# Kernel optimization log

Measured on AMD Instinct MI355X. Metric: run time of the kernel, lower is better.

## Reference

```python
import jax, jax.numpy as jnp
import numpy as np

B, N, IN_F, OUT_F, H = 64, 256, 128, 128, 4
NEG_SLOPE = 0.2  # nn.LeakyReLU(dropout) -> slope 0.2


def setup_inputs() -> dict:
    key = jax.random.key(0)
    ks = jax.random.split(key, 10)
    h = jax.random.normal(ks[0], (B, N, IN_F), dtype=jnp.float32)
    projection_matrix = jax.random.normal(ks[1], (B, N, N), dtype=jnp.float32)
    similarity_matrix = jax.random.uniform(ks[2], (B, N, N), dtype=jnp.float32) * 2.0 - 1.0
    quadrant_matrix = jax.random.randint(ks[3], (B, N, N, 2), 0, 4, dtype=jnp.int32)
    # parameters (xavier-ish scaling)
    W = jax.random.normal(ks[4], (IN_F, OUT_F * H), dtype=jnp.float32) / np.sqrt(IN_F)
    a = jax.random.normal(ks[5], (H, 2 * OUT_F, 1), dtype=jnp.float32) / np.sqrt(2 * OUT_F)
    w_proj = jax.random.normal(ks[6], (OUT_F,), dtype=jnp.float32) / np.sqrt(OUT_F)
    w_sim = jax.random.normal(ks[7], (OUT_F,), dtype=jnp.float32) / np.sqrt(OUT_F)
    quadrant_bias = jax.random.normal(ks[8], (4, 4), dtype=jnp.float32) * 0.02
    W_concat = jax.random.normal(ks[9], (OUT_F * H, OUT_F), dtype=jnp.float32) / np.sqrt(OUT_F * H)
    return {"h": h, "projection_matrix": projection_matrix,
            "similarity_matrix": similarity_matrix, "quadrant_matrix": quadrant_matrix,
            "W": W, "a": a, "w_proj": w_proj, "w_sim": w_sim,
            "quadrant_bias": quadrant_bias, "W_concat": W_concat}


def reference(h, projection_matrix, similarity_matrix, quadrant_matrix,
              W, a, w_proj, w_sim, quadrant_bias, W_concat):
    b, n, _ = h.shape
    # Wh_heads: (B, H, N, F)
    Wh = (h @ W).reshape(b, n, H, OUT_F).transpose(0, 2, 1, 3)
    # GAT score: a^T [Wh_i || Wh_j] decomposes into two rank-1 terms
    a1, a2 = a[:, :OUT_F, 0], a[:, OUT_F:, 0]            # (H, F) each
    e_i = jnp.einsum('bhnf,hf->bhn', Wh, a1)
    e_j = jnp.einsum('bhnf,hf->bhn', Wh, a2)
    e = e_i[:, :, :, None] + e_j[:, :, None, :]          # (B, H, N, N)
    e = jnp.where(e > 0, e, NEG_SLOPE * e)               # leaky relu
    # projection bias: <Wh_i, proj[b,i,j] * w_proj> = (Wh_i . w_proj) * proj[b,i,j]
    s_proj = jnp.einsum('bhnf,f->bhn', Wh, w_proj)
    e = e + s_proj[:, :, :, None] * projection_matrix[:, None, :, :]
    # similarity bias, same factored form
    s_sim = jnp.einsum('bhnf,f->bhn', Wh, w_sim)
    e = e + s_sim[:, :, :, None] * similarity_matrix[:, None, :, :]
    # quadrant bias gather
    qb = quadrant_bias[quadrant_matrix[..., 0], quadrant_matrix[..., 1]]  # (B, N, N)
    e = e + qb[:, None, :, :]
    attn = jax.nn.softmax(e, axis=-1)                    # dropout is identity in eval
    h_prime = jnp.einsum('bhij,bhjf->bhif', attn, Wh)    # (B, H, N, F)
    h_prime = h_prime.transpose(0, 2, 1, 3).reshape(b, n, H * OUT_F) @ W_concat
    return jax.nn.elu(h_prime)
```

## Files before the change

### kernel.cpp

```cpp
#include <hip/hip_runtime.h>
#include <math.h>

#define BB 64
#define NN 256
#define IN_F 128
#define OF 128
#define HH 4
#define NEG_SLOPE 0.2f

typedef __attribute__((ext_vector_type(8))) short short8;
typedef __attribute__((ext_vector_type(4))) float f32x4;

#define MFMA16(a, b, c) __builtin_amdgcn_mfma_f32_16x16x32_bf16(a, b, c, 0, 0, 0)

__device__ inline unsigned short f2bf(float x) {
    unsigned u = __float_as_uint(x);
    u += 0x7fff + ((u >> 16) & 1);
    return (unsigned short)(u >> 16);
}

__global__ __launch_bounds__(256) void k0_convert(const float* __restrict__ h,
        const float* __restrict__ W, const float* __restrict__ Wc,
        unsigned short* __restrict__ h_bf, unsigned short* __restrict__ Wt,
        unsigned short* __restrict__ Wct) {
    int blk = blockIdx.x, t = threadIdx.x;
    if (blk < 2048) {
        int idx = blk * 256 + t;
        float4 v = ((const float4*)h)[idx];
        ushort4 o;
        o.x = f2bf(v.x); o.y = f2bf(v.y); o.z = f2bf(v.z); o.w = f2bf(v.w);
        ((ushort4*)h_bf)[idx] = o;
    } else if (blk < 2064) {
        int base = (blk - 2048) * 4096 + t * 16;
#pragma unroll
        for (int e = 0; e < 16; e++) {
            int idx = base + e;
            int f = idx >> 7, k = idx & 127;
            Wt[idx] = f2bf(W[k * 512 + f]);
        }
    } else {
        int base = (blk - 2064) * 4096 + t * 16;
#pragma unroll
        for (int e = 0; e < 16; e++) {
            int idx = base + e;
            int c = idx >> 9, k = idx & 511;
            Wct[idx] = f2bf(Wc[k * 128 + c]);
        }
    }
}

__global__ __launch_bounds__(256) void k1_wh(const unsigned short* __restrict__ h_bf,
        const unsigned short* __restrict__ Wt, const float* __restrict__ a,
        const float* __restrict__ w_proj, const float* __restrict__ w_sim,
        unsigned short* __restrict__ Wht, float* __restrict__ ei,
        float* __restrict__ ej, float* __restrict__ sp, float* __restrict__ ss) {
    __shared__ float a1s[512], a2s[512], wps[128], wss[128];
    int blk = blockIdx.x;
    int b = blk >> 2;
    int n0 = (blk & 3) * 64;
    int t = threadIdx.x;
    for (int idx = t; idx < 512; idx += 256) {
        int hh = idx >> 7, f = idx & 127;
        a1s[idx] = a[hh * 256 + f];
        a2s[idx] = a[hh * 256 + 128 + f];
    }
    if (t < 128) { wps[t] = w_proj[t]; wss[t] = w_sim[t]; }
    __syncthreads();

    int w = t >> 6, lane = t & 63;
    int cc = lane & 15, g = lane >> 4;

    short8 bh[4][4];
#pragma unroll
    for (int tn = 0; tn < 4; tn++)
#pragma unroll
        for (int ks = 0; ks < 4; ks++)
            bh[tn][ks] = *(const short8*)(h_bf +
                ((size_t)(b * NN + n0 + tn * 16 + cc)) * IN_F + ks * 32 + g * 8);

    f32x4 acc[8][4];
#pragma unroll
    for (int tf = 0; tf < 8; tf++)
#pragma unroll
        for (int tn = 0; tn < 4; tn++) acc[tf][tn] = (f32x4)(0.f);

#pragma unroll
    for (int tf = 0; tf < 8; tf++) {
        short8 aw[4];
#pragma unroll
        for (int ks = 0; ks < 4; ks++)
            aw[ks] = *(const short8*)(Wt +
                (size_t)(w * 128 + tf * 16 + cc) * IN_F + ks * 32 + g * 8);
#pragma unroll
        for (int tn = 0; tn < 4; tn++)
#pragma unroll
            for (int ks = 0; ks < 4; ks++)
                acc[tf][tn] = MFMA16(aw[ks], bh[tn][ks], acc[tf][tn]);
    }

    unsigned short* whb = Wht + (size_t)(b * HH + w) * OF * NN;
#pragma unroll
    for (int tf = 0; tf < 8; tf++)
#pragma unroll
        for (int r = 0; r < 4; r++) {
            int f = tf * 16 + g * 4 + r;
#pragma unroll
            for (int tn = 0; tn < 4; tn++)
                whb[(size_t)f * NN + n0 + tn * 16 + cc] = f2bf(acc[tf][tn][r]);
        }

#pragma unroll
    for (int tn = 0; tn < 4; tn++) {
        float q0 = 0.f, q1 = 0.f, q2 = 0.f, q3 = 0.f;
#pragma unroll
        for (int tf = 0; tf < 8; tf++)
#pragma unroll
            for (int r = 0; r < 4; r++) {
                float v = acc[tf][tn][r];
                int f = tf * 16 + g * 4 + r;
                q0 += v * a1s[w * 128 + f];
                q1 += v * a2s[w * 128 + f];
                q2 += v * wps[f];
                q3 += v * wss[f];
            }
        q0 += __shfl_xor(q0, 16); q0 += __shfl_xor(q0, 32);
        q1 += __shfl_xor(q1, 16); q1 += __shfl_xor(q1, 32);
        q2 += __shfl_xor(q2, 16); q2 += __shfl_xor(q2, 32);
        q3 += __shfl_xor(q3, 16); q3 += __shfl_xor(q3, 32);
        if (g == 0) {
            size_t idx = (size_t)(b * HH + w) * NN + n0 + tn * 16 + cc;
            ei[idx] = q0; ej[idx] = q1; sp[idx] = q2; ss[idx] = q3;
        }
    }
}

__global__ __launch_bounds__(256) void k2_fused(
        const float* __restrict__ proj, const float* __restrict__ sim,
        const int* __restrict__ qm, const float* __restrict__ qbias,
        const float* __restrict__ ei, const float* __restrict__ ej,
        const float* __restrict__ sp, const float* __restrict__ ss,
        const unsigned short* __restrict__ Wht, const unsigned short* __restrict__ Wct,
        float* __restrict__ out) {
    __shared__ __align__(16) char at_lds[32768];
    __shared__ __align__(16) char hp_lds[16384];
    __shared__ float eis[HH][16], sps[HH][16], sss[HH][16];
    __shared__ float qb_s[16];
    float* ejs = (float*)hp_lds;

    int blk = blockIdx.x;
    int b = blk >> 4;
    int i0 = (blk & 15) * 16;
    int t = threadIdx.x;
    int wave = t >> 6, lane = t & 63;

    for (int c = t; c < HH * NN; c += 256)
        ejs[c] = ej[(size_t)b * HH * NN + c];
    if (t < 64) {
        int hh = t >> 4, ii = t & 15;
        size_t base = ((size_t)b * HH + hh) * NN + i0 + ii;
        eis[hh][ii] = ei[base]; sps[hh][ii] = sp[base]; sss[hh][ii] = ss[base];
    }
    if (t < 16) qb_s[t] = qbias[t];
    __syncthreads();

    int j0 = lane * 4;
    for (int rr = 0; rr < 4; rr++) {
        int ii = wave * 4 + rr;
        int i = i0 + ii;
        size_t rb = ((size_t)b * NN + i) * NN + j0;
        float4 P4 = *(const float4*)&proj[rb];
        float4 S4 = *(const float4*)&sim[rb];
        int4 q0 = *(const int4*)&qm[rb * 2];
        int4 q1 = *(const int4*)&qm[rb * 2 + 4];
        float qb0 = qb_s[q0.x * 4 + q0.y], qb1 = qb_s[q0.z * 4 + q0.w];
        float qb2 = qb_s[q1.x * 4 + q1.y], qb3 = qb_s[q1.z * 4 + q1.w];
        float e[HH][4];
#pragma unroll
        for (int hh = 0; hh < HH; hh++) {
            float4 ej4 = *(const float4*)&ejs[hh * 256 + j0];
            float bi = eis[hh][ii], spv = sps[hh][ii], ssv = sss[hh][ii];
            float x;
            x = bi + ej4.x; x = x > 0.f ? x : NEG_SLOPE * x; e[hh][0] = x + spv * P4.x + ssv * S4.x + qb0;
            x = bi + ej4.y; x = x > 0.f ? x : NEG_SLOPE * x; e[hh][1] = x + spv * P4.y + ssv * S4.y + qb1;
            x = bi + ej4.z; x = x > 0.f ? x : NEG_SLOPE * x; e[hh][2] = x + spv * P4.z + ssv * S4.z + qb2;
            x = bi + ej4.w; x = x > 0.f ? x : NEG_SLOPE * x; e[hh][3] = x + spv * P4.w + ssv * S4.w + qb3;
        }
        float m[HH];
#pragma unroll
        for (int hh = 0; hh < HH; hh++)
            m[hh] = fmaxf(fmaxf(e[hh][0], e[hh][1]), fmaxf(e[hh][2], e[hh][3]));
#pragma unroll
        for (int off = 32; off; off >>= 1)
#pragma unroll
            for (int hh = 0; hh < HH; hh++)
                m[hh] = fmaxf(m[hh], __shfl_xor(m[hh], off));
        float s[HH];
#pragma unroll
        for (int hh = 0; hh < HH; hh++) {
            e[hh][0] = __expf(e[hh][0] - m[hh]);
            e[hh][1] = __expf(e[hh][1] - m[hh]);
            e[hh][2] = __expf(e[hh][2] - m[hh]);
            e[hh][3] = __expf(e[hh][3] - m[hh]);
            s[hh] = (e[hh][0] + e[hh][1]) + (e[hh][2] + e[hh][3]);
        }
#pragma unroll
        for (int off = 32; off; off >>= 1)
#pragma unroll
            for (int hh = 0; hh < HH; hh++) s[hh] += __shfl_xor(s[hh], off);
#pragma unroll
        for (int hh = 0; hh < HH; hh++) {
            float inv = 1.0f / s[hh];
            ushort4 pk;
            pk.x = f2bf(e[hh][0] * inv);
            pk.y = f2bf(e[hh][1] * inv);
            pk.z = f2bf(e[hh][2] * inv);
            pk.w = f2bf(e[hh][3] * inv);
            int off2 = hh * 8192 + ii * 512 + ((j0 * 2) ^ ((ii & 7) << 4));
            *(ushort4*)(at_lds + off2) = pk;
        }
    }
    __syncthreads();

    int w = wave;
    int row = lane & 15, g = lane >> 4;
    short8 af[8];
#pragma unroll
    for (int ks = 0; ks < 8; ks++) {
        int off = w * 8192 + row * 512 + ((((ks * 32 + g * 8) * 2)) ^ ((row & 7) << 4));
        af[ks] = *(const short8*)(at_lds + off);
    }
    f32x4 acc[8];
#pragma unroll
    for (int ft = 0; ft < 8; ft++) acc[ft] = (f32x4)(0.f);
    const unsigned short* whb = Wht + (size_t)(b * HH + w) * OF * NN;
#pragma unroll
    for (int ft = 0; ft < 8; ft++) {
        const unsigned short* wb = whb + (size_t)(ft * 16 + row) * NN + g * 8;
#pragma unroll
        for (int ks = 0; ks < 8; ks++) {
            short8 bf = *(const short8*)(wb + ks * 32);
            acc[ft] = MFMA16(af[ks], bf, acc[ft]);
        }
    }
#pragma unroll
    for (int ft = 0; ft < 8; ft++)
#pragma unroll
        for (int r = 0; r < 4; r++) {
            int i = g * 4 + r;
            int kf = w * 128 + ft * 16 + row;
            int off = i * 1024 + ((kf * 2) ^ ((i & 7) << 4));
            *(unsigned short*)(hp_lds + off) = f2bf(acc[ft][r]);
        }
    __syncthreads();

    short8 ah[16];
#pragma unroll
    for (int ks = 0; ks < 16; ks++) {
        int off = row * 1024 + (((ks * 32 + g * 8) * 2) ^ ((row & 7) << 4));
        ah[ks] = *(const short8*)(hp_lds + off);
    }
    f32x4 o2[2];
    o2[0] = (f32x4)(0.f); o2[1] = (f32x4)(0.f);
#pragma unroll
    for (int ct = 0; ct < 2; ct++) {
        int c = (w * 2 + ct) * 16 + row;
        const unsigned short* wc = Wct + (size_t)c * 512 + g * 8;
#pragma unroll
        for (int ks = 0; ks < 16; ks++) {
            short8 bf = *(const short8*)(wc + ks * 32);
            o2[ct] = MFMA16(ah[ks], bf, o2[ct]);
        }
    }
#pragma unroll
    for (int ct = 0; ct < 2; ct++)
#pragma unroll
        for (int r = 0; r < 4; r++) {
            float v = o2[ct][r];
            v = v > 0.f ? v : expm1f(v);
            int i = i0 + g * 4 + r;
            int c = (w * 2 + ct) * 16 + row;
            out[((size_t)b * NN + i) * OF + c] = v;
        }
}

extern "C" void kernel_launch(void* const* d_in, const int* in_sizes, int n_in,
                              void* d_out, int out_size, void* d_ws, size_t ws_size,
                              hipStream_t stream) {
    const float* h      = (const float*)d_in[0];
    const float* proj   = (const float*)d_in[1];
    const float* sim    = (const float*)d_in[2];
    const int*   qm     = (const int*)d_in[3];
    const float* W      = (const float*)d_in[4];
    const float* a      = (const float*)d_in[5];
    const float* w_proj = (const float*)d_in[6];
    const float* w_sim  = (const float*)d_in[7];
    const float* qbias  = (const float*)d_in[8];
    const float* Wc     = (const float*)d_in[9];
    float* out = (float*)d_out;

    unsigned short* h_bf = (unsigned short*)d_ws;
    unsigned short* Wt   = h_bf + (size_t)BB * NN * IN_F;
    unsigned short* Wct  = Wt + 512 * 128;
    unsigned short* Wht  = Wct + 128 * 512;
    float* ei = (float*)(Wht + (size_t)BB * HH * OF * NN);
    float* ej = ei + (size_t)BB * HH * NN;
    float* sp = ej + (size_t)BB * HH * NN;
    float* ss = sp + (size_t)BB * HH * NN;

    k0_convert<<<2080, 256, 0, stream>>>(h, W, Wc, h_bf, Wt, Wct);
    k1_wh<<<BB * 4, 256, 0, stream>>>(h_bf, Wt, a, w_proj, w_sim, Wht, ei, ej, sp, ss);
    k2_fused<<<BB * 16, 256, 0, stream>>>(proj, sim, qm, qbias, ei, ej, sp, ss, Wht, Wct, out);
}
```

Before: 182.4 us.

## Coalesce weight transposes, remap blocks across XCDs, prefetch k2 inputs, shrink k1 registers

The weight transpose-convert in k0 now stages 16-row slabs of W and W_concat in shared memory. It then writes contiguous 16-element bf16 runs, replacing the strided scalar reads. k1 and k2 remap block indices so that all blocks for one batch land on the same XCD, which should improve L2 locality. k1 no longer keeps a full 8x4 accumulator array, computing the per-tile dot products and stores inside the tf loop, which lowers register pressure. k2 issues all four rows' proj/sim/quadrant loads up front to increase memory-level parallelism, at the cost of more live registers.

```diff
diff --git a/kernel.cpp b/kernel.cpp
--- a/kernel.cpp
+++ b/kernel.cpp
@@ -23,6 +23,7 @@
         const float* __restrict__ W, const float* __restrict__ Wc,
         unsigned short* __restrict__ h_bf, unsigned short* __restrict__ Wt,
         unsigned short* __restrict__ Wct) {
+    __shared__ float hl[16][516];
     int blk = blockIdx.x, t = threadIdx.x;
     if (blk < 2048) {
         int idx = blk * 256 + t;
@@ -30,21 +31,48 @@
         ushort4 o;
         o.x = f2bf(v.x); o.y = f2bf(v.y); o.z = f2bf(v.z); o.w = f2bf(v.w);
         ((ushort4*)h_bf)[idx] = o;
-    } else if (blk < 2064) {
-        int base = (blk - 2048) * 4096 + t * 16;
-#pragma unroll
-        for (int e = 0; e < 16; e++) {
-            int idx = base + e;
-            int f = idx >> 7, k = idx & 127;
-            Wt[idx] = f2bf(W[k * 512 + f]);
+    } else if (blk < 2056) {
+        int k0 = (blk - 2048) * 16;
+#pragma unroll
+        for (int it = 0; it < 8; it++) {
+            int li = it * 256 + t;
+            int row = li >> 7, col4 = li & 127;
+            float4 v = ((const float4*)(W + (size_t)(k0 + row) * 512))[col4];
+            *(float4*)&hl[row][col4 * 4] = v;
+        }
+        __syncthreads();
+#pragma unroll
+        for (int cc = 0; cc < 2; cc++) {
+            int c = t * 2 + cc;
+            short8 s0, s1;
+#pragma unroll
+            for (int k = 0; k < 8; k++) s0[k] = (short)f2bf(hl[k][c]);
+#pragma unroll
+            for (int k = 0; k < 8; k++) s1[k] = (short)f2bf(hl[k + 8][c]);
+            unsigned short* dst = Wt + (size_t)c * 128 + k0;
+            *(short8*)dst = s0;
+            *(short8*)(dst + 8) = s1;
         }
     } else {
-        int base = (blk - 2064) * 4096 + t * 16;
-#pragma unroll
-        for (int e = 0; e < 16; e++) {
-            int idx = base + e;
-            int c = idx >> 9, k = idx & 511;
-            Wct[idx] = f2bf(Wc[k * 128 + c]);
+        int k0 = (blk - 2056) * 16;
+#pragma unroll
+        for (int it = 0; it < 2; it++) {
+            int li = it * 256 + t;
+            int row = li >> 5, col4 = li & 31;
+            float4 v = ((const float4*)(Wc + (size_t)(k0 + row) * 128))[col4];
+            *(float4*)&hl[row][col4 * 4] = v;
+        }
+        __syncthreads();
+        if (t < 128) {
+            int c = t;
+            short8 s0, s1;
+#pragma unroll
+            for (int k = 0; k < 8; k++) s0[k] = (short)f2bf(hl[k][c]);
+#pragma unroll
+            for (int k = 0; k < 8; k++) s1[k] = (short)f2bf(hl[k + 8][c]);
+            unsigned short* dst = Wct + (size_t)c * 512 + k0;
+            *(short8*)dst = s0;
+            *(short8*)(dst + 8) = s1;
         }
     }
 }
@@ -55,9 +83,10 @@
         unsigned short* __restrict__ Wht, float* __restrict__ ei,
         float* __restrict__ ej, float* __restrict__ sp, float* __restrict__ ss) {
     __shared__ float a1s[512], a2s[512], wps[128], wss[128];
-    int blk = blockIdx.x;
-    int b = blk >> 2;
-    int n0 = (blk & 3) * 64;
+    int l = blockIdx.x;
+    int xcd = l & 7, m = l >> 3;
+    int b = xcd + ((m >> 2) << 3);
+    int n0 = (m & 3) * 64;
     int t = threadIdx.x;
     for (int idx = t; idx < 512; idx += 256) {
         int hh = idx >> 7, f = idx & 127;
@@ -78,11 +107,9 @@
             bh[tn][ks] = *(const short8*)(h_bf +
                 ((size_t)(b * NN + n0 + tn * 16 + cc)) * IN_F + ks * 32 + g * 8);
 
-    f32x4 acc[8][4];
-#pragma unroll
-    for (int tf = 0; tf < 8; tf++)
-#pragma unroll
-        for (int tn = 0; tn < 4; tn++) acc[tf][tn] = (f32x4)(0.f);
+    float q0[4] = {0.f,0.f,0.f,0.f}, q1[4] = {0.f,0.f,0.f,0.f};
+    float q2[4] = {0.f,0.f,0.f,0.f}, q3[4] = {0.f,0.f,0.f,0.f};
+    unsigned short* whb = Wht + (size_t)(b * HH + w) * OF * NN;
 
 #pragma unroll
     for (int tf = 0; tf < 8; tf++) {
@@ -91,45 +118,47 @@
         for (int ks = 0; ks < 4; ks++)
             aw[ks] = *(const short8*)(Wt +
                 (size_t)(w * 128 + tf * 16 + cc) * IN_F + ks * 32 + g * 8);
+        f32x4 acc[4];
+#pragma unroll
+        for (int tn = 0; tn < 4; tn++) acc[tn] = (f32x4)(0.f);
 #pragma unroll
         for (int tn = 0; tn < 4; tn++)
 #pragma unroll
             for (int ks = 0; ks < 4; ks++)
-                acc[tf][tn] = MFMA16(aw[ks], bh[tn][ks], acc[tf][tn]);
-    }
-
-    unsigned short* whb = Wht + (size_t)(b * HH + w) * OF * NN;
-#pragma unroll
-    for (int tf = 0; tf < 8; tf++)
+                acc[tn] = MFMA16(aw[ks], bh[tn][ks], acc[tn]);
+
+        float a1v[4], a2v[4], wpv[4], wsv[4];
 #pragma unroll
         for (int r = 0; r < 4; r++) {
             int f = tf * 16 + g * 4 + r;
-#pragma unroll
-            for (int tn = 0; tn < 4; tn++)
-                whb[(size_t)f * NN + n0 + tn * 16 + cc] = f2bf(acc[tf][tn][r]);
-        }
+            a1v[r] = a1s[w * 128 + f];
+            a2v[r] = a2s[w * 128 + f];
+            wpv[r] = wps[f];
+            wsv[r] = wss[f];
+        }
+#pragma unroll
+        for (int tn = 0; tn < 4; tn++)
+#pragma unroll
+            for (int r = 0; r < 4; r++) {
+                float v = acc[tn][r];
+                q0[tn] += v * a1v[r];
+                q1[tn] += v * a2v[r];
+                q2[tn] += v * wpv[r];
+                q3[tn] += v * wsv[r];
+                whb[(size_t)(tf * 16 + g * 4 + r) * NN + n0 + tn * 16 + cc] = f2bf(v);
+            }
+    }
 
 #pragma unroll
     for (int tn = 0; tn < 4; tn++) {
-        float q0 = 0.f, q1 = 0.f, q2 = 0.f, q3 = 0.f;
-#pragma unroll
-        for (int tf = 0; tf < 8; tf++)
-#pragma unroll
-            for (int r = 0; r < 4; r++) {
-                float v = acc[tf][tn][r];
-                int f = tf * 16 + g * 4 + r;
-                q0 += v * a1s[w * 128 + f];
-                q1 += v * a2s[w * 128 + f];
-                q2 += v * wps[f];
-                q3 += v * wss[f];
-            }
-        q0 += __shfl_xor(q0, 16); q0 += __shfl_xor(q0, 32);
-        q1 += __shfl_xor(q1, 16); q1 += __shfl_xor(q1, 32);
-        q2 += __shfl_xor(q2, 16); q2 += __shfl_xor(q2, 32);
-        q3 += __shfl_xor(q3, 16); q3 += __shfl_xor(q3, 32);
+        float p0 = q0[tn], p1 = q1[tn], p2 = q2[tn], p3 = q3[tn];
+        p0 += __shfl_xor(p0, 16); p0 += __shfl_xor(p0, 32);
+        p1 += __shfl_xor(p1, 16); p1 += __shfl_xor(p1, 32);
+        p2 += __shfl_xor(p2, 16); p2 += __shfl_xor(p2, 32);
+        p3 += __shfl_xor(p3, 16); p3 += __shfl_xor(p3, 32);
         if (g == 0) {
             size_t idx = (size_t)(b * HH + w) * NN + n0 + tn * 16 + cc;
-            ei[idx] = q0; ej[idx] = q1; sp[idx] = q2; ss[idx] = q3;
+            ei[idx] = p0; ej[idx] = p1; sp[idx] = p2; ss[idx] = p3;
         }
     }
 }
@@ -147,9 +176,10 @@
     __shared__ float qb_s[16];
     float* ejs = (float*)hp_lds;
 
-    int blk = blockIdx.x;
-    int b = blk >> 4;
-    int i0 = (blk & 15) * 16;
+    int l = blockIdx.x;
+    int xcd = l & 7, m = l >> 3;
+    int b = xcd + ((m >> 4) << 3);
+    int i0 = (m & 15) * 16;
     int t = threadIdx.x;
     int wave = t >> 6, lane = t & 63;
 
@@ -164,43 +194,49 @@
     __syncthreads();
 
     int j0 = lane * 4;
+    float4 P4[4], S4[4];
+    int4 qa[4], qc[4];
+#pragma unroll
+    for (int rr = 0; rr < 4; rr++) {
+        int i = i0 + wave * 4 + rr;
+        size_t rb = ((size_t)b * NN + i) * NN + j0;
+        P4[rr] = *(const float4*)&proj[rb];
+        S4[rr] = *(const float4*)&sim[rb];
+        qa[rr] = *(const int4*)&qm[rb * 2];
+        qc[rr] = *(const int4*)&qm[rb * 2 + 4];
+    }
+#pragma unroll
     for (int rr = 0; rr < 4; rr++) {
         int ii = wave * 4 + rr;
-        int i = i0 + ii;
-        size_t rb = ((size_t)b * NN + i) * NN + j0;
-        float4 P4 = *(const float4*)&proj[rb];
-        float4 S4 = *(const float4*)&sim[rb];
-        int4 q0 = *(const int4*)&qm[rb * 2];
-        int4 q1 = *(const int4*)&qm[rb * 2 + 4];
-        float qb0 = qb_s[q0.x * 4 + q0.y], qb1 = qb_s[q0.z * 4 + q0.w];
-        float qb2 = qb_s[q1.x * 4 + q1.y], qb3 = qb_s[q1.z * 4 + q1.w];
+        float qb0 = qb_s[qa[rr].x * 4 + qa[rr].y], qb1 = qb_s[qa[rr].z * 4 + qa[rr].w];
+        float qb2 = qb_s[qc[rr].x * 4 + qc[rr].y], qb3 = qb_s[qc[rr].z * 4 + qc[rr].w];
         float e[HH][4];
 #pragma unroll
         for (int hh = 0; hh < HH; hh++) {
             float4 ej4 = *(const float4*)&ejs[hh * 256 + j0];
             float bi = eis[hh][ii], spv = sps[hh][ii], ssv = sss[hh][ii];
             float x;
-            x = bi + ej4.x; x = x > 0.f ? x : NEG_SLOPE * x; e[hh][0] = x + spv * P4.x + ssv * S4.x + qb0;
-            x = bi + ej4.y; x = x > 0.f ? x : NEG_SLOPE * x; e[hh][1] = x + spv * P4.y + ssv * S4.y + qb1;
-            x = bi + ej4.z; x = x > 0.f ? x : NEG_SLOPE * x; e[hh][2] = x + spv * P4.z + ssv * S4.z + qb2;
-            x = bi + ej4.w; x = x > 0.f ? x : NEG_SLOPE * x; e[hh][3] = x + spv * P4.w + ssv * S4.w + qb3;
-        }
-        float m[HH];
+            x = bi + ej4.x; x = x > 0.f ? x : NEG_SLOPE * x; e[hh][0] = x + spv * P4[rr].x + ssv * S4[rr].x + qb0;
+            x = bi + ej4.y; x = x > 0.f ? x : NEG_SLOPE * x; e[hh][1] = x + spv * P4[rr].y + ssv * S4[rr].y + qb1;
+            x = bi + ej4.z; x = x > 0.f ? x : NEG_SLOPE * x; e[hh][2] = x + spv * P4[rr].z + ssv * S4[rr].z + qb2;
+            x = bi + ej4.w; x = x > 0.f ? x : NEG_SLOPE * x; e[hh][3] = x + spv * P4[rr].w + ssv * S4[rr].w + qb3;
+        }
+        float mx[HH];
 #pragma unroll
         for (int hh = 0; hh < HH; hh++)
-            m[hh] = fmaxf(fmaxf(e[hh][0], e[hh][1]), fmaxf(e[hh][2], e[hh][3]));
+            mx[hh] = fmaxf(fmaxf(e[hh][0], e[hh][1]), fmaxf(e[hh][2], e[hh][3]));
 #pragma unroll
         for (int off = 32; off; off >>= 1)
 #pragma unroll
             for (int hh = 0; hh < HH; hh++)
-                m[hh] = fmaxf(m[hh], __shfl_xor(m[hh], off));
+                mx[hh] = fmaxf(mx[hh], __shfl_xor(mx[hh], off));
         float s[HH];
 #pragma unroll
         for (int hh = 0; hh < HH; hh++) {
-            e[hh][0] = __expf(e[hh][0] - m[hh]);
-            e[hh][1] = __expf(e[hh][1] - m[hh]);
-            e[hh][2] = __expf(e[hh][2] - m[hh]);
-            e[hh][3] = __expf(e[hh][3] - m[hh]);
+            e[hh][0] = __expf(e[hh][0] - mx[hh]);
+            e[hh][1] = __expf(e[hh][1] - mx[hh]);
+            e[hh][2] = __expf(e[hh][2] - mx[hh]);
+            e[hh][3] = __expf(e[hh][3] - mx[hh]);
             s[hh] = (e[hh][0] + e[hh][1]) + (e[hh][2] + e[hh][3]);
         }
 #pragma unroll
@@ -307,7 +343,7 @@
     float* sp = ej + (size_t)BB * HH * NN;
     float* ss = sp + (size_t)BB * HH * NN;
 
-    k0_convert<<<2080, 256, 0, stream>>>(h, W, Wc, h_bf, Wt, Wct);
+    k0_convert<<<2088, 256, 0, stream>>>(h, W, Wc, h_bf, Wt, Wct);
     k1_wh<<<BB * 4, 256, 0, stream>>>(h_bf, Wt, a, w_proj, w_sim, Wht, ei, ej, sp, ss);
     k2_fused<<<BB * 16, 256, 0, stream>>>(proj, sim, qm, qbias, ei, ej, sp, ss, Wht, Wct, out);
 }
```

New measurement: 185.0 us. Within noise of the previous version (+1.4%).
